# Optimization experiments

Hardware: AMD Instinct MI355X
Metric: run time of the kernel (lower is better)

The kernel has to match this reference:

```python
import jax, jax.numpy as jnp
import numpy as np
from jax import lax

N_INPUT, N_HIDDEN, N_OUTPUT = 1024, 2048, 1024
T, B = 512, 64

def setup_inputs() -> dict:
    key = jax.random.key(0)
    k_x, k_ih, k_hh, k_out = jax.random.split(key, 4)
    stdv = 1.0 / np.sqrt(N_HIDDEN)
    xs = jax.random.normal(k_x, (T, B, N_INPUT), dtype=jnp.float32)
    # torch nn.Linear weights are [out_features, in_features], init U(-stdv, stdv)
    W_ih = jax.random.uniform(k_ih, (N_HIDDEN, N_INPUT), jnp.float32, -stdv, stdv)
    W_hh = jax.random.uniform(k_hh, (N_HIDDEN, N_HIDDEN), jnp.float32, -stdv, stdv)
    W_out = jax.random.uniform(k_out, (N_OUTPUT, N_HIDDEN), jnp.float32, -stdv, stdv)
    return {"xs": xs, "W_ih": W_ih, "W_hh": W_hh, "W_out": W_out}

def reference(xs, W_ih, W_hh, W_out):
    # xs: [T, B, n_input] time-major. state starts as None -> relu(W_ih x),
    # which equals relu(W_ih x + W_hh * 0), so h0 = zeros is exact.
    n_hidden = W_hh.shape[0]
    h0 = jnp.zeros((xs.shape[1], n_hidden), dtype=xs.dtype)

    def step(h, x):
        h = jax.nn.relu(x @ W_ih.T + h @ W_hh.T)  # [B, n_hidden]
        return h, h

    _, h_seq = lax.scan(step, h0, xs)        # [T, B, n_hidden]
    ys = h_seq @ W_out.T                     # [T, B, n_output]
    return jnp.transpose(ys, (1, 0, 2))      # [B, T, n_output] (transpose(0,1))
```

## Files before the change

kernel.cpp:

```cpp
#include <hip/hip_runtime.h>
#include <hip/hip_bf16.h>
#include <stdint.h>


#define TT 512
#define BB 64
#define NIN 1024
#define NH 2048
#define NOUT 1024

typedef __attribute__((ext_vector_type(8))) short bf8;
typedef __attribute__((ext_vector_type(4))) float f4;
typedef __attribute__((ext_vector_type(4))) unsigned int u4;

static __device__ __forceinline__ unsigned short f2bf(float f) {
  __hip_bfloat16 h = __float2bfloat16(f);
  return __builtin_bit_cast(unsigned short, h);
}
static __device__ __forceinline__ float bf2f(unsigned short v) {
  return __bfloat162float(__builtin_bit_cast(__hip_bfloat16, v));
}
static __device__ __forceinline__ u4 pack8(const float* f) {
  u4 r;
#pragma unroll
  for (int i = 0; i < 4; ++i) {
    unsigned lo = f2bf(f[2 * i]);
    unsigned hi = f2bf(f[2 * i + 1]);
    r[i] = lo | (hi << 16);
  }
  return r;
}

static __device__ __forceinline__ size_t sl_idx(int m, int col) {
  return (((size_t)(m >> 6) * 128 + (col >> 4)) << 10) + (size_t)(m & 63) * 16 + (col & 15);
}

template <bool ABF, bool TRANS>
__global__ void gemm_bt(const void* __restrict__ Av, const float* __restrict__ Bw,
                        void* __restrict__ Cv, int M, int N, int K) {
  constexpr int BM = 128, BN = 128, BK = 32;
  __shared__ u4 As[BM * 4];
  __shared__ u4 Bs[BN * 4];
  const int nt = N / BN;
  const int mi = (int)blockIdx.x / nt;
  const int ni = (int)blockIdx.x % nt;
  const int m0 = mi * BM, n0 = ni * BN;
  const int t = threadIdx.x;
  const int l = t & 63, w = t >> 6, wr = w >> 1, wc = w & 1;
  const int lr = l & 15, lq = l >> 4;

  f4 acc[4][4] = {};

  const int srow = t >> 1;
  const int sc0 = (t & 1) * 2;

  for (int kt = 0; kt < K; kt += BK) {
    if (ABF) {
      const unsigned short* A = (const unsigned short*)Av;
#pragma unroll
      for (int cc = 0; cc < 2; ++cc) {
        int c = sc0 + cc;
        u4 v = *(const u4*)(A + sl_idx(m0 + srow, kt + c * 8));
        As[srow * 4 + (c ^ ((srow ^ (srow >> 2)) & 3))] = v;
      }
    } else {
      const float* A = (const float*)Av;
#pragma unroll
      for (int cc = 0; cc < 2; ++cc) {
        int c = sc0 + cc;
        const float* p = A + (size_t)(m0 + srow) * K + kt + c * 8;
        float4 v0 = *(const float4*)p;
        float4 v1 = *(const float4*)(p + 4);
        float f[8] = {v0.x, v0.y, v0.z, v0.w, v1.x, v1.y, v1.z, v1.w};
        As[srow * 4 + (c ^ ((srow ^ (srow >> 2)) & 3))] = pack8(f);
      }
    }
#pragma unroll
    for (int cc = 0; cc < 2; ++cc) {
      int c = sc0 + cc;
      const float* p = Bw + (size_t)(n0 + srow) * K + kt + c * 8;
      float4 v0 = *(const float4*)p;
      float4 v1 = *(const float4*)(p + 4);
      float f[8] = {v0.x, v0.y, v0.z, v0.w, v1.x, v1.y, v1.z, v1.w};
      Bs[srow * 4 + (c ^ ((srow ^ (srow >> 2)) & 3))] = pack8(f);
    }
    __syncthreads();

    bf8 a[4], b[4];
#pragma unroll
    for (int i = 0; i < 4; ++i) {
      int ra = wr * 64 + i * 16 + lr;
      a[i] = __builtin_bit_cast(bf8, As[ra * 4 + (lq ^ ((ra ^ (ra >> 2)) & 3))]);
      int rb = wc * 64 + i * 16 + lr;
      b[i] = __builtin_bit_cast(bf8, Bs[rb * 4 + (lq ^ ((rb ^ (rb >> 2)) & 3))]);
    }
#pragma unroll
    for (int i = 0; i < 4; ++i)
#pragma unroll
      for (int j = 0; j < 4; ++j)
        acc[i][j] = __builtin_amdgcn_mfma_f32_16x16x32_bf16(a[i], b[j], acc[i][j], 0, 0, 0);
    __syncthreads();
  }

  if (TRANS) {
    float* C = (float*)Cv;
#pragma unroll
    for (int i = 0; i < 4; ++i)
#pragma unroll
      for (int j = 0; j < 4; ++j)
#pragma unroll
        for (int r = 0; r < 4; ++r) {
          int m = m0 + wr * 64 + i * 16 + lq * 4 + r;
          int n = n0 + wc * 64 + j * 16 + lr;
          C[(size_t)(m & 63) * (TT * NOUT) + (size_t)(m >> 6) * NOUT + n] = acc[i][j][r];
        }
  } else {
    unsigned short* C = (unsigned short*)Cv;
#pragma unroll
    for (int i = 0; i < 4; ++i)
#pragma unroll
      for (int j = 0; j < 4; ++j)
#pragma unroll
        for (int r = 0; r < 4; ++r) {
          int m = m0 + wr * 64 + i * 16 + lq * 4 + r;
          int n = n0 + wc * 64 + j * 16 + lr;
          C[sl_idx(m, n)] = f2bf(acc[i][j][r]);
        }
  }
}

__global__ __launch_bounds__(1024, 4) void rnn_recur(unsigned short* __restrict__ hseq,
                                                     const float* __restrict__ Whh,
                                                     unsigned* __restrict__ flags) {
  __shared__ u4 Wl[16 * 256];
  __shared__ float red[2][8][32][20];
  const int t = threadIdx.x;
  const int jb = (int)blockIdx.x & 127;
  const int bh = (int)blockIdx.x >> 7;
  const int j0 = jb * 16;

  {
    const int jl = t >> 6;
    const int c0 = (t & 63) * 4;
#pragma unroll
    for (int c = 0; c < 4; ++c) {
      int cc = c0 + c;
      const float* p = Whh + (size_t)(j0 + jl) * NH + cc * 8;
      float4 v0 = *(const float4*)p;
      float4 v1 = *(const float4*)(p + 4);
      float f[8] = {v0.x, v0.y, v0.z, v0.w, v1.x, v1.y, v1.z, v1.w};
      Wl[jl * 256 + (cc ^ (jl & 7))] = pack8(f);
    }
  }

  const int l = t & 63, w = t >> 6;
  const int lr = l & 15, lq = l >> 4;
  const int bg = w & 1, kg = w >> 1;
  const int row = bh * 32 + bg * 16 + lr;

  const int wrowL = bg * 16 + (l >> 2);
  const int wjq = l & 3;
  const size_t woff = (size_t)(bh * 32 + wrowL) * 16 + wjq * 4;

  unsigned long long pre = 0;

  __syncthreads();

  if (w < 2) {
    size_t e0 = ((size_t)jb << 10) + woff;
    unsigned long long p0 = *(const unsigned long long*)(hseq + e0);
    unsigned long long hv = 0;
#pragma unroll
    for (int i = 0; i < 4; ++i) {
      unsigned long long x = (p0 >> (16 * i)) & 0xffffull;
      if (!(x & 0x8000ull)) hv |= x << (16 * i);
    }
    __hip_atomic_store((unsigned long long*)(hseq + e0), hv, __ATOMIC_RELAXED,
                       __HIP_MEMORY_SCOPE_AGENT);
    asm volatile("s_waitcnt vmcnt(0)" ::: "memory");
    if (l == 0)
      __hip_atomic_store(flags + ((int)blockIdx.x * 2 + w), 1u, __ATOMIC_RELAXED,
                         __HIP_MEMORY_SCOPE_AGENT);
    pre = __hip_atomic_load(
        (const unsigned long long*)(hseq + (((size_t)128 + jb) << 10) + woff),
        __ATOMIC_RELAXED, __HIP_MEMORY_SCOPE_AGENT);
  }

  for (int ts = 1; ts < TT; ++ts) {
    {
      const unsigned* fp = flags + ((bh * 128 + kg * 16 + lr) * 2 + bg);
      long spins = 0;
      for (;;) {
        unsigned fv = __hip_atomic_load(fp, __ATOMIC_RELAXED, __HIP_MEMORY_SCOPE_AGENT);
        if (__ballot(fv >= (unsigned)ts) == ~0ull) break;
        __builtin_amdgcn_s_sleep(1);
        if (++spins > (1L << 22)) break;
      }
    }
    asm volatile("" ::: "memory");

    const size_t tb = (size_t)(ts - 1) * 128;
    const size_t rowoff = (size_t)row * 16 + (lq & 1) * 8;
    const size_t sbase = tb + kg * 16 + (lq >> 1);
    unsigned long long ad[8];
#pragma unroll
    for (int u = 0; u < 8; ++u)
      ad[u] = (unsigned long long)(uintptr_t)(hseq + (((sbase + 2 * u) << 10) + rowoff));
    u4 av[8];
    asm volatile(
        "global_load_dwordx4 %0, %8, off\n\t"
        "global_load_dwordx4 %1, %9, off\n\t"
        "global_load_dwordx4 %2, %10, off\n\t"
        "global_load_dwordx4 %3, %11, off\n\t"
        "global_load_dwordx4 %4, %12, off\n\t"
        "global_load_dwordx4 %5, %13, off\n\t"
        "global_load_dwordx4 %6, %14, off\n\t"
        "global_load_dwordx4 %7, %15, off\n\t"
        "s_waitcnt vmcnt(0)"
        : "=&v"(av[0]), "=&v"(av[1]), "=&v"(av[2]), "=&v"(av[3]),
          "=&v"(av[4]), "=&v"(av[5]), "=&v"(av[6]), "=&v"(av[7])
        : "v"(ad[0]), "v"(ad[1]), "v"(ad[2]), "v"(ad[3]),
          "v"(ad[4]), "v"(ad[5]), "v"(ad[6]), "v"(ad[7])
        : "memory");

    f4 acc0 = {}, acc1 = {};
#pragma unroll
    for (int u = 0; u < 8; ++u) {
      bf8 af = __builtin_bit_cast(bf8, av[u]);
      int c = kg * 32 + u * 4 + lq;
      bf8 bfr = __builtin_bit_cast(bf8, Wl[lr * 256 + (c ^ (lr & 7))]);
      if (u & 1)
        acc1 = __builtin_amdgcn_mfma_f32_16x16x32_bf16(af, bfr, acc1, 0, 0, 0);
      else
        acc0 = __builtin_amdgcn_mfma_f32_16x16x32_bf16(af, bfr, acc0, 0, 0, 0);
    }
    f4 a2 = acc0 + acc1;

    const int buf = ts & 1;
#pragma unroll
    for (int r = 0; r < 4; ++r) red[buf][kg][bg * 16 + lq * 4 + r][lr] = a2[r];
    __syncthreads();

    if (w < 2) {
      f4 s = {};
#pragma unroll
      for (int q = 0; q < 8; ++q) s += *(const f4*)&red[buf][q][wrowL][wjq * 4];
      float sf[4];
#pragma unroll
      for (int i = 0; i < 4; ++i) {
        float v = s[i] + bf2f((unsigned short)((pre >> (16 * i)) & 0xffffull));
        sf[i] = v > 0.f ? v : 0.f;
      }
      unsigned lo = (unsigned)f2bf(sf[0]) | ((unsigned)f2bf(sf[1]) << 16);
      unsigned hi = (unsigned)f2bf(sf[2]) | ((unsigned)f2bf(sf[3]) << 16);
      unsigned long long hv = (unsigned long long)lo | ((unsigned long long)hi << 32);
      size_t eo = (((size_t)ts * 128 + jb) << 10) + woff;
      __hip_atomic_store((unsigned long long*)(hseq + eo), hv, __ATOMIC_RELAXED,
                         __HIP_MEMORY_SCOPE_AGENT);
      asm volatile("s_waitcnt vmcnt(0)" ::: "memory");
      if (l == 0)
        __hip_atomic_store(flags + ((int)blockIdx.x * 2 + w), (unsigned)(ts + 1),
                           __ATOMIC_RELAXED, __HIP_MEMORY_SCOPE_AGENT);
      if (ts + 1 < TT)
        pre = __hip_atomic_load(
            (const unsigned long long*)(hseq + (((size_t)(ts + 1) * 128 + jb) << 10) + woff),
            __ATOMIC_RELAXED, __HIP_MEMORY_SCOPE_AGENT);
    }
  }
}

__global__ void kinit(unsigned* f) { f[threadIdx.x] = 0u; }

extern "C" void kernel_launch(void* const* d_in, const int* in_sizes, int n_in,
                              void* d_out, int out_size, void* d_ws, size_t ws_size,
                              hipStream_t stream) {
  const float* xs = (const float*)d_in[0];
  const float* Wih = (const float*)d_in[1];
  const float* Whh = (const float*)d_in[2];
  const float* Wout = (const float*)d_in[3];

  unsigned short* hseq = (unsigned short*)d_ws;
  unsigned* flags = (unsigned*)((char*)d_ws + (size_t)TT * BB * NH * 2);

  kinit<<<1, 512, 0, stream>>>(flags);

  gemm_bt<false, false><<<(TT * BB / 128) * (NH / 128), 256, 0, stream>>>(
      (const void*)xs, Wih, (void*)hseq, TT * BB, NH, NIN);

  rnn_recur<<<256, 1024, 0, stream>>>(hseq, Whh, flags);

  gemm_bt<true, true><<<(TT * BB / 128) * (NOUT / 128), 256, 0, stream>>>(
      (const void*)hseq, Wout, d_out, TT * BB, NOUT, NH);
}
```

Baseline: 4.153 ms.

## Repartition RNN recurrence into 4 batch groups with 32-column blocks and new layout

The persistent recurrence kernel now splits the batch into 4 groups of 16 rows, with each block owning 32 hidden columns. Previously it used 2 groups of 32 rows with 16 columns per block. The hidden-state scratch layout changes to 16x32 tiles so each wave reads contiguous 1KB chunks with immediate offsets. Loads use sc0/sc1 to bypass caches, and the epilogue raises wave priority. The goal is to shrink per-step latency by reducing the flag fan-in (32 producers per group) and the address computation. The cost is twice the W_hh slice held in LDS per block and more MFMAs per wave.

```diff
diff --git a/kernel.cpp b/kernel.cpp
--- a/kernel.cpp
+++ b/kernel.cpp
@@ -32,7 +32,8 @@
 }
 
 static __device__ __forceinline__ size_t sl_idx(int m, int col) {
-  return (((size_t)(m >> 6) * 128 + (col >> 4)) << 10) + (size_t)(m & 63) * 16 + (col & 15);
+  return ((((size_t)(m >> 6) * 4 + ((m & 63) >> 4)) * 64 + (col >> 5)) << 9) +
+         (size_t)((m & 63) & 15) * 32 + (col & 31);
 }
 
 template <bool ABF, bool TRANS>
@@ -129,22 +130,23 @@
   }
 }
 
-__global__ __launch_bounds__(1024, 4) void rnn_recur(unsigned short* __restrict__ hseq,
-                                                     const float* __restrict__ Whh,
-                                                     unsigned* __restrict__ flags) {
-  __shared__ u4 Wl[16 * 256];
-  __shared__ float red[2][8][32][20];
+__global__ __launch_bounds__(512, 2) void rnn_recur(unsigned short* __restrict__ hseq,
+                                                    const float* __restrict__ Whh,
+                                                    unsigned* __restrict__ flags) {
+  __shared__ u4 Wl[32 * 256];
+  __shared__ float red[2][4][16][36];
   const int t = threadIdx.x;
-  const int jb = (int)blockIdx.x & 127;
-  const int bh = (int)blockIdx.x >> 7;
-  const int j0 = jb * 16;
+  const int bid = (int)blockIdx.x;
+  const int g = (bid & 7) >> 1;
+  const int jb = ((bid >> 3) << 1) | (bid & 1);
+  const int j0 = jb * 32;
 
   {
-    const int jl = t >> 6;
-    const int c0 = (t & 63) * 4;
-#pragma unroll
-    for (int c = 0; c < 4; ++c) {
-      int cc = c0 + c;
+    const int jl = t >> 4;
+    const int ci = t & 15;
+#pragma unroll
+    for (int q = 0; q < 16; ++q) {
+      int cc = ci * 16 + q;
       const float* p = Whh + (size_t)(j0 + jl) * NH + cc * 8;
       float4 v0 = *(const float4*)p;
       float4 v1 = *(const float4*)(p + 4);
@@ -155,43 +157,48 @@
 
   const int l = t & 63, w = t >> 6;
   const int lr = l & 15, lq = l >> 4;
-  const int bg = w & 1, kg = w >> 1;
-  const int row = bh * 32 + bg * 16 + lr;
-
-  const int wrowL = bg * 16 + (l >> 2);
+  const int kg = w >> 1, jh = w & 1;
+
+  char* hb = (char*)hseq;
+  const size_t gofs = (size_t)g << 16;
+
+  const int wr_r = l >> 2;
   const int wjq = l & 3;
-  const size_t woff = (size_t)(bh * 32 + wrowL) * 16 + wjq * 4;
+  const size_t wbyte = (size_t)wr_r * 64 + jh * 32 + wjq * 8;
 
   unsigned long long pre = 0;
 
   __syncthreads();
 
   if (w < 2) {
-    size_t e0 = ((size_t)jb << 10) + woff;
-    unsigned long long p0 = *(const unsigned long long*)(hseq + e0);
+    size_t e0 = (gofs + ((size_t)jb << 10)) + wbyte;
+    unsigned long long p0 = __hip_atomic_load((const unsigned long long*)(hb + e0),
+                                              __ATOMIC_RELAXED, __HIP_MEMORY_SCOPE_AGENT);
     unsigned long long hv = 0;
 #pragma unroll
     for (int i = 0; i < 4; ++i) {
       unsigned long long x = (p0 >> (16 * i)) & 0xffffull;
       if (!(x & 0x8000ull)) hv |= x << (16 * i);
     }
-    __hip_atomic_store((unsigned long long*)(hseq + e0), hv, __ATOMIC_RELAXED,
+    __hip_atomic_store((unsigned long long*)(hb + e0), hv, __ATOMIC_RELAXED,
                        __HIP_MEMORY_SCOPE_AGENT);
     asm volatile("s_waitcnt vmcnt(0)" ::: "memory");
     if (l == 0)
-      __hip_atomic_store(flags + ((int)blockIdx.x * 2 + w), 1u, __ATOMIC_RELAXED,
+      __hip_atomic_store(flags + ((g * 64 + jb) * 2 + w), 1u, __ATOMIC_RELAXED,
                          __HIP_MEMORY_SCOPE_AGENT);
     pre = __hip_atomic_load(
-        (const unsigned long long*)(hseq + (((size_t)128 + jb) << 10) + woff),
+        (const unsigned long long*)(hb + ((size_t)(1 * 4) << 16) + gofs + ((size_t)jb << 10) + wbyte),
         __ATOMIC_RELAXED, __HIP_MEMORY_SCOPE_AGENT);
   }
 
   for (int ts = 1; ts < TT; ++ts) {
     {
-      const unsigned* fp = flags + ((bh * 128 + kg * 16 + lr) * 2 + bg);
+      const unsigned* fp = flags + ((g * 64 + kg * 16 + (l >> 1)) * 2 + (l & 1));
       long spins = 0;
       for (;;) {
-        unsigned fv = __hip_atomic_load(fp, __ATOMIC_RELAXED, __HIP_MEMORY_SCOPE_AGENT);
+        unsigned fv = (l < 32) ? __hip_atomic_load(fp, __ATOMIC_RELAXED,
+                                                   __HIP_MEMORY_SCOPE_AGENT)
+                               : 0xffffffffu;
         if (__ballot(fv >= (unsigned)ts) == ~0ull) break;
         __builtin_amdgcn_s_sleep(1);
         if (++spins > (1L << 22)) break;
@@ -199,52 +206,61 @@
     }
     asm volatile("" ::: "memory");
 
-    const size_t tb = (size_t)(ts - 1) * 128;
-    const size_t rowoff = (size_t)row * 16 + (lq & 1) * 8;
-    const size_t sbase = tb + kg * 16 + (lq >> 1);
-    unsigned long long ad[8];
-#pragma unroll
-    for (int u = 0; u < 8; ++u)
-      ad[u] = (unsigned long long)(uintptr_t)(hseq + (((sbase + 2 * u) << 10) + rowoff));
-    u4 av[8];
+    const size_t rowoff = (size_t)(l & 15) * 64 + (size_t)(l >> 4) * 16;
+    const size_t base = (((size_t)(ts - 1) * 4) << 16) + gofs + ((size_t)(kg * 16) << 10) + rowoff;
+    unsigned long long a0 = (unsigned long long)(uintptr_t)(hb + base);
+    unsigned long long a1 = a0 + 4096;
+    unsigned long long a2 = a0 + 8192;
+    unsigned long long a3 = a0 + 12288;
+    u4 av[16];
     asm volatile(
-        "global_load_dwordx4 %0, %8, off\n\t"
-        "global_load_dwordx4 %1, %9, off\n\t"
-        "global_load_dwordx4 %2, %10, off\n\t"
-        "global_load_dwordx4 %3, %11, off\n\t"
-        "global_load_dwordx4 %4, %12, off\n\t"
-        "global_load_dwordx4 %5, %13, off\n\t"
-        "global_load_dwordx4 %6, %14, off\n\t"
-        "global_load_dwordx4 %7, %15, off\n\t"
+        "global_load_dwordx4 %0, %16, off sc0 sc1\n\t"
+        "global_load_dwordx4 %1, %16, off offset:1024 sc0 sc1\n\t"
+        "global_load_dwordx4 %2, %16, off offset:2048 sc0 sc1\n\t"
+        "global_load_dwordx4 %3, %16, off offset:3072 sc0 sc1\n\t"
+        "global_load_dwordx4 %4, %17, off sc0 sc1\n\t"
+        "global_load_dwordx4 %5, %17, off offset:1024 sc0 sc1\n\t"
+        "global_load_dwordx4 %6, %17, off offset:2048 sc0 sc1\n\t"
+        "global_load_dwordx4 %7, %17, off offset:3072 sc0 sc1\n\t"
+        "global_load_dwordx4 %8, %18, off sc0 sc1\n\t"
+        "global_load_dwordx4 %9, %18, off offset:1024 sc0 sc1\n\t"
+        "global_load_dwordx4 %10, %18, off offset:2048 sc0 sc1\n\t"
+        "global_load_dwordx4 %11, %18, off offset:3072 sc0 sc1\n\t"
+        "global_load_dwordx4 %12, %19, off sc0 sc1\n\t"
+        "global_load_dwordx4 %13, %19, off offset:1024 sc0 sc1\n\t"
+        "global_load_dwordx4 %14, %19, off offset:2048 sc0 sc1\n\t"
+        "global_load_dwordx4 %15, %19, off offset:3072 sc0 sc1\n\t"
         "s_waitcnt vmcnt(0)"
         : "=&v"(av[0]), "=&v"(av[1]), "=&v"(av[2]), "=&v"(av[3]),
-          "=&v"(av[4]), "=&v"(av[5]), "=&v"(av[6]), "=&v"(av[7])
-        : "v"(ad[0]), "v"(ad[1]), "v"(ad[2]), "v"(ad[3]),
-          "v"(ad[4]), "v"(ad[5]), "v"(ad[6]), "v"(ad[7])
+          "=&v"(av[4]), "=&v"(av[5]), "=&v"(av[6]), "=&v"(av[7]),
+          "=&v"(av[8]), "=&v"(av[9]), "=&v"(av[10]), "=&v"(av[11]),
+          "=&v"(av[12]), "=&v"(av[13]), "=&v"(av[14]), "=&v"(av[15])
+        : "v"(a0), "v"(a1), "v"(a2), "v"(a3)
         : "memory");
 
     f4 acc0 = {}, acc1 = {};
 #pragma unroll
-    for (int u = 0; u < 8; ++u) {
-      bf8 af = __builtin_bit_cast(bf8, av[u]);
-      int c = kg * 32 + u * 4 + lq;
-      bf8 bfr = __builtin_bit_cast(bf8, Wl[lr * 256 + (c ^ (lr & 7))]);
-      if (u & 1)
+    for (int c = 0; c < 16; ++c) {
+      bf8 af = __builtin_bit_cast(bf8, av[c]);
+      int ci = kg * 64 + c * 4 + lq;
+      bf8 bfr = __builtin_bit_cast(bf8, Wl[(jh * 16 + lr) * 256 + (ci ^ (lr & 7))]);
+      if (c & 1)
         acc1 = __builtin_amdgcn_mfma_f32_16x16x32_bf16(af, bfr, acc1, 0, 0, 0);
       else
         acc0 = __builtin_amdgcn_mfma_f32_16x16x32_bf16(af, bfr, acc0, 0, 0, 0);
     }
-    f4 a2 = acc0 + acc1;
+    f4 a2v = acc0 + acc1;
 
     const int buf = ts & 1;
 #pragma unroll
-    for (int r = 0; r < 4; ++r) red[buf][kg][bg * 16 + lq * 4 + r][lr] = a2[r];
+    for (int i = 0; i < 4; ++i) red[buf][kg][(l >> 4) * 4 + i][jh * 16 + (l & 15)] = a2v[i];
     __syncthreads();
 
     if (w < 2) {
+      __builtin_amdgcn_s_setprio(1);
       f4 s = {};
 #pragma unroll
-      for (int q = 0; q < 8; ++q) s += *(const f4*)&red[buf][q][wrowL][wjq * 4];
+      for (int q = 0; q < 4; ++q) s += *(const f4*)&red[buf][q][wr_r][jh * 16 + wjq * 4];
       float sf[4];
 #pragma unroll
       for (int i = 0; i < 4; ++i) {
@@ -254,17 +270,19 @@
       unsigned lo = (unsigned)f2bf(sf[0]) | ((unsigned)f2bf(sf[1]) << 16);
       unsigned hi = (unsigned)f2bf(sf[2]) | ((unsigned)f2bf(sf[3]) << 16);
       unsigned long long hv = (unsigned long long)lo | ((unsigned long long)hi << 32);
-      size_t eo = (((size_t)ts * 128 + jb) << 10) + woff;
-      __hip_atomic_store((unsigned long long*)(hseq + eo), hv, __ATOMIC_RELAXED,
+      size_t eo = (((size_t)ts * 4) << 16) + gofs + ((size_t)jb << 10) + wbyte;
+      __hip_atomic_store((unsigned long long*)(hb + eo), hv, __ATOMIC_RELAXED,
                          __HIP_MEMORY_SCOPE_AGENT);
       asm volatile("s_waitcnt vmcnt(0)" ::: "memory");
       if (l == 0)
-        __hip_atomic_store(flags + ((int)blockIdx.x * 2 + w), (unsigned)(ts + 1),
+        __hip_atomic_store(flags + ((g * 64 + jb) * 2 + w), (unsigned)(ts + 1),
                            __ATOMIC_RELAXED, __HIP_MEMORY_SCOPE_AGENT);
       if (ts + 1 < TT)
         pre = __hip_atomic_load(
-            (const unsigned long long*)(hseq + (((size_t)(ts + 1) * 128 + jb) << 10) + woff),
+            (const unsigned long long*)(hb + (((size_t)(ts + 1) * 4) << 16) + gofs +
+                                        ((size_t)jb << 10) + wbyte),
             __ATOMIC_RELAXED, __HIP_MEMORY_SCOPE_AGENT);
+      __builtin_amdgcn_s_setprio(0);
     }
   }
 }
@@ -287,7 +305,7 @@
   gemm_bt<false, false><<<(TT * BB / 128) * (NH / 128), 256, 0, stream>>>(
       (const void*)xs, Wih, (void*)hseq, TT * BB, NH, NIN);
 
-  rnn_recur<<<256, 1024, 0, stream>>>(hseq, Whh, flags);
+  rnn_recur<<<256, 512, 0, stream>>>(hseq, Whh, flags);
 
   gemm_bt<true, true><<<(TT * BB / 128) * (NOUT / 128), 256, 0, stream>>>(
       (const void*)hseq, Wout, d_out, TT * BB, NOUT, NH);
```

After: 3.946 ms. 1.05x faster.
